# Kernel optimization log

Measured on AMD Instinct MI355X. Metric: run time of the kernel, lower is better.

Reference implementation:

```python
import jax, jax.numpy as jnp
import numpy as np

N_NODES = 50000
N_EDGES = 800000
NFEAT = 128
NHID = 128
BN_EPS = 1e-5


def setup_inputs() -> dict:
    key = jax.random.key(0)
    ks = jax.random.split(key, 8)
    x = jax.random.normal(ks[0], (N_NODES, NFEAT), dtype=jnp.float32)
    edge_index = jax.random.randint(ks[1], (2, N_EDGES), 0, N_NODES, dtype=jnp.int64)
    # Linear weights in torch layout [out, in]; scaled like kaiming-ish init.
    W1 = jax.random.normal(ks[2], (NHID, NFEAT), dtype=jnp.float32) / np.sqrt(NFEAT)
    b1 = jax.random.normal(ks[3], (NHID,), dtype=jnp.float32) * 0.01
    gamma = jnp.ones((NHID,), dtype=jnp.float32)
    beta = jnp.zeros((NHID,), dtype=jnp.float32)
    W2 = jax.random.normal(ks[4], (NHID, NHID), dtype=jnp.float32) / np.sqrt(NHID)
    b2 = jax.random.normal(ks[5], (NHID,), dtype=jnp.float32) * 0.01
    return {"x": x, "edge_index": edge_index, "W1": W1, "b1": b1,
            "gamma": gamma, "beta": beta, "W2": W2, "b2": b2}


def reference(x, edge_index, W1, b1, gamma, beta, W2, b2):
    # GINConv, eps = 0: h = (1 + eps) * x + sum_{j in N(i)} x_j
    src, dst = edge_index[0], edge_index[1]
    agg = x + jax.ops.segment_sum(x[src], dst, num_segments=N_NODES)  # [N, nfeat]
    # MLP: Linear -> ReLU -> BatchNorm1d (training stats) -> Linear
    h = jnp.maximum(agg @ W1.T + b1, 0.0)                             # [N, nhid]
    mean = jnp.mean(h, axis=0)
    var = jnp.var(h, axis=0)  # biased variance, as torch BN uses for normalization
    h = (h - mean) * jax.lax.rsqrt(var + BN_EPS) * gamma + beta
    return h @ W2.T + b2
```

## Files before the change

### kernel.cpp

```cpp
#include <hip/hip_runtime.h>

#define N_NODES 50000
#define N_EDGES 800000
#define NF 128
#define BN_EPS 1e-5f
#define G_ROWS 32
#define GBLOCKS ((N_NODES + G_ROWS - 1) / G_ROWS)
#define NB 1568
#define AP 136
#define HP 132
#define CAP 32
#define OVFCAP 8192

typedef __attribute__((ext_vector_type(8))) short short8;
typedef __attribute__((ext_vector_type(4))) float f32x4;

__device__ __forceinline__ unsigned short f2bf(float f) {
    union { float f; unsigned int i; } v; v.f = f;
    unsigned int r = (v.i + 0x7fffu + ((v.i >> 16) & 1u)) >> 16;
    return (unsigned short)r;
}
__device__ __forceinline__ float bf2f(unsigned short u) {
    union { unsigned int i; float f; } v; v.i = ((unsigned int)u) << 16; return v.f;
}
__device__ __forceinline__ float bflo(unsigned int u) { return bf2f((unsigned short)(u & 0xffffu)); }
__device__ __forceinline__ float bfhi(unsigned int u) { return bf2f((unsigned short)(u >> 16)); }

#define SETUP_C (N_NODES * NF / 4)
#define SETUP_P (128 * 128)

__global__ void scatter_build(const int* __restrict__ ei,
                              int* __restrict__ counts, int* __restrict__ ovfcnt,
                              int* __restrict__ ovf, int* __restrict__ bucket,
                              const float* __restrict__ x, unsigned short* __restrict__ xb,
                              const float* __restrict__ W1, const float* __restrict__ W2,
                              unsigned short* __restrict__ Wb1, unsigned short* __restrict__ Wb2,
                              int do_convert) {
    int i = blockIdx.x * blockDim.x + threadIdx.x;
    if (!do_convert && i >= N_EDGES) i += SETUP_C;
    if (i < N_EDGES) {
        int dst = ei[N_EDGES + i];
        int src = ei[i];
        int k = atomicAdd(&counts[dst], 1);
        if (k < CAP) {
            bucket[dst * CAP + k] = src;
        } else {
            int o = atomicAdd(ovfcnt, 1);
            if (o < OVFCAP) { ovf[2 * o] = dst; ovf[2 * o + 1] = src; }
        }
    } else if (i < N_EDGES + SETUP_C) {
        int j = i - N_EDGES;
        float4 v = ((const float4*)x)[j];
        ushort4 u;
        u.x = f2bf(v.x); u.y = f2bf(v.y); u.z = f2bf(v.z); u.w = f2bf(v.w);
        ((ushort4*)xb)[j] = u;
    } else if (i < N_EDGES + SETUP_C + SETUP_P) {
        int j = i - N_EDGES - SETUP_C;
        Wb1[j] = f2bf(W1[j]);
        Wb2[j] = f2bf(W2[j]);
    }
}

__global__ __launch_bounds__(256, 6) void fused_gather_gemm1_bf16(
    const unsigned short* __restrict__ xb,
    const int* __restrict__ counts,
    const int* __restrict__ bucket,
    const int* __restrict__ ovfcnt,
    const int* __restrict__ ovf,
    const unsigned short* __restrict__ Wb,
    const float* __restrict__ b1,
    unsigned short* __restrict__ buf,
    float* __restrict__ P) {
    __shared__ __align__(16) char smem[G_ROWS * HP * 4];
    unsigned short (*At)[AP] = (unsigned short (*)[AP])smem;
    float (*Ht)[HP] = (float (*)[HP])smem;

    int t = threadIdx.x;
    int wave = t >> 6, lane = t & 63;
    int base = blockIdx.x * G_ROWS;
    int nrows = N_NODES - base; if (nrows > G_ROWS) nrows = G_ROWS;

    const unsigned int* x2 = (const unsigned int*)xb;
    int novf = *ovfcnt; if (novf > OVFCAP) novf = OVFCAP;

    for (int nn = 0; nn < 8; nn++) {
        int r = wave * 8 + nn;
        int node = base + r;
        unsigned int packed = 0u;
        if (node < N_NODES) {
            unsigned int u = x2[(size_t)node * 64 + lane];
            float ax = bflo(u), ay = bfhi(u);
            int deg = counts[node];
            int cnt = deg < CAP ? deg : CAP;
            const int* bkt = bucket + (size_t)node * CAP;
            int e = 0;
            for (; e + 15 < cnt; e += 16) {
                unsigned int uu[16];
#pragma unroll
                for (int k = 0; k < 16; k++) uu[k] = x2[(size_t)bkt[e + k] * 64 + lane];
#pragma unroll
                for (int k = 0; k < 16; k++) { ax += bflo(uu[k]); ay += bfhi(uu[k]); }
            }
            for (; e + 3 < cnt; e += 4) {
                unsigned int u0 = x2[(size_t)bkt[e] * 64 + lane];
                unsigned int u1 = x2[(size_t)bkt[e + 1] * 64 + lane];
                unsigned int u2 = x2[(size_t)bkt[e + 2] * 64 + lane];
                unsigned int u3 = x2[(size_t)bkt[e + 3] * 64 + lane];
                ax += bflo(u0) + bflo(u1) + bflo(u2) + bflo(u3);
                ay += bfhi(u0) + bfhi(u1) + bfhi(u2) + bfhi(u3);
            }
            for (; e < cnt; e++) {
                unsigned int u0 = x2[(size_t)bkt[e] * 64 + lane];
                ax += bflo(u0);
                ay += bfhi(u0);
            }
            if (deg > CAP) {
                for (int o = 0; o < novf; o++) {
                    if (ovf[2 * o] == node) {
                        unsigned int u0 = x2[(size_t)ovf[2 * o + 1] * 64 + lane];
                        ax += bflo(u0);
                        ay += bfhi(u0);
                    }
                }
            }
            packed = ((unsigned int)f2bf(ay) << 16) | (unsigned int)f2bf(ax);
        }
        ((unsigned int*)&At[r][0])[lane] = packed;
    }
    __syncthreads();

    int m0 = (wave & 1) * 16;
    int n0 = (wave >> 1) * 64;
    int l15 = lane & 15, q = lane >> 4;

    f32x4 acc[4];
#pragma unroll
    for (int i = 0; i < 4; i++) acc[i] = (f32x4){0.f, 0.f, 0.f, 0.f};

#pragma unroll
    for (int kc = 0; kc < 4; kc++) {
        short8 a = *((const short8*)&At[m0 + l15][kc * 32 + q * 8]);
#pragma unroll
        for (int tile = 0; tile < 4; tile++) {
            short8 b = *((const short8*)(Wb + (size_t)(n0 + 16 * tile + l15) * 128 + kc * 32 + q * 8));
            acc[tile] = __builtin_amdgcn_mfma_f32_16x16x32_bf16(a, b, acc[tile], 0, 0, 0);
        }
    }
    __syncthreads();

#pragma unroll
    for (int tile = 0; tile < 4; tile++) {
        int col = n0 + 16 * tile + l15;
        float bias = b1[col];
#pragma unroll
        for (int reg = 0; reg < 4; reg++) {
            int row = q * 4 + reg;
            Ht[m0 + row][col] = fmaxf(acc[tile][reg] + bias, 0.f);
        }
    }
    __syncthreads();

    for (int i = t; i < G_ROWS * 32; i += 256) {
        int r = i >> 5, c4 = i & 31;
        int row = base + r;
        if (row < N_NODES) {
            float4 v = *((const float4*)&Ht[r][c4 * 4]);
            ushort4 u;
            u.x = f2bf(v.x); u.y = f2bf(v.y); u.z = f2bf(v.z); u.w = f2bf(v.w);
            *((ushort4*)(buf + (size_t)row * NF + c4 * 4)) = u;
        }
    }

    {
        int f = t & 127;
        bool issq = (t >= 128);
        float s = 0.f;
        for (int r = 0; r < nrows; r++) {
            float v = Ht[r][f];
            s += issq ? v * v : v;
        }
        P[(size_t)t * NB + blockIdx.x] = s;
    }
}

__global__ __launch_bounds__(256) void bn_reduce(const float* __restrict__ P,
                                                 const float* __restrict__ gamma,
                                                 const float* __restrict__ beta,
                                                 float* __restrict__ ab) {
    __shared__ float s1[256], s2[256];
    int f = blockIdx.x;
    int j = threadIdx.x;
    float a = 0.f, b = 0.f;
    for (int k = j; k < GBLOCKS; k += 256) {
        a += P[(size_t)f * NB + k];
        b += P[(size_t)(128 + f) * NB + k];
    }
    s1[j] = a; s2[j] = b;
    __syncthreads();
    for (int off = 128; off > 0; off >>= 1) {
        if (j < off) { s1[j] += s1[j + off]; s2[j] += s2[j + off]; }
        __syncthreads();
    }
    if (j == 0) {
        float mean = s1[0] * (1.0f / N_NODES);
        float var = s2[0] * (1.0f / N_NODES) - mean * mean;
        float rstd = rsqrtf(var + BN_EPS);
        float aa = gamma[f] * rstd;
        float cc = beta[f] - mean * aa;
        ab[f] = aa;
        ab[128 + f] = cc;
    }
}

__global__ __launch_bounds__(256) void gemm2_bf16(
    const unsigned short* __restrict__ buf,
    const unsigned short* __restrict__ Wb,
    const float* __restrict__ b2,
    const float* __restrict__ ab,
    float* __restrict__ out) {
    __shared__ __align__(16) char smem[G_ROWS * HP * 4];
    unsigned short (*At)[AP] = (unsigned short (*)[AP])smem;
    float (*Ht)[HP] = (float (*)[HP])smem;

    int t = threadIdx.x;
    int base = blockIdx.x * G_ROWS;
    int nrows = N_NODES - base; if (nrows > G_ROWS) nrows = G_ROWS;

    for (int i = t; i < G_ROWS * 32; i += 256) {
        int r = i >> 5, c4 = i & 31;
        ushort4 u = make_ushort4(0, 0, 0, 0);
        if (r < nrows) {
            ushort4 hv = *((const ushort4*)(buf + (size_t)(base + r) * NF + c4 * 4));
            float4 av = ((const float4*)ab)[c4];
            float4 cv = ((const float4*)(ab + 128))[c4];
            u.x = f2bf(bf2f(hv.x) * av.x + cv.x);
            u.y = f2bf(bf2f(hv.y) * av.y + cv.y);
            u.z = f2bf(bf2f(hv.z) * av.z + cv.z);
            u.w = f2bf(bf2f(hv.w) * av.w + cv.w);
        }
        *((ushort4*)&At[r][c4 * 4]) = u;
    }
    __syncthreads();

    int wave = t >> 6, lane = t & 63;
    int m0 = (wave & 1) * 16;
    int n0 = (wave >> 1) * 64;
    int l15 = lane & 15, q = lane >> 4;

    f32x4 acc[4];
#pragma unroll
    for (int i = 0; i < 4; i++) acc[i] = (f32x4){0.f, 0.f, 0.f, 0.f};

#pragma unroll
    for (int kc = 0; kc < 4; kc++) {
        short8 a = *((const short8*)&At[m0 + l15][kc * 32 + q * 8]);
#pragma unroll
        for (int tile = 0; tile < 4; tile++) {
            short8 b = *((const short8*)(Wb + (size_t)(n0 + 16 * tile + l15) * 128 + kc * 32 + q * 8));
            acc[tile] = __builtin_amdgcn_mfma_f32_16x16x32_bf16(a, b, acc[tile], 0, 0, 0);
        }
    }
    __syncthreads();

#pragma unroll
    for (int tile = 0; tile < 4; tile++) {
        int col = n0 + 16 * tile + l15;
        float bias = b2[col];
#pragma unroll
        for (int reg = 0; reg < 4; reg++) {
            int row = q * 4 + reg;
            Ht[m0 + row][col] = acc[tile][reg] + bias;
        }
    }
    __syncthreads();

    for (int i = t; i < G_ROWS * 32; i += 256) {
        int r = i >> 5, c4 = i & 31;
        int row = base + r;
        if (row < N_NODES)
            *((float4*)(out + (size_t)row * NF + c4 * 4)) = *((const float4*)&Ht[r][c4 * 4]);
    }
}

__global__ void finalize_bn(const float* __restrict__ stats,
                            const float* __restrict__ gamma,
                            const float* __restrict__ beta,
                            float* __restrict__ ab) {
    int f = threadIdx.x;
    if (f < 128) {
        float mean = stats[f] * (1.0f / N_NODES);
        float var = stats[128 + f] * (1.0f / N_NODES) - mean * mean;
        float rstd = rsqrtf(var + BN_EPS);
        float a = gamma[f] * rstd;
        float c = beta[f] - mean * a;
        ab[f] = a;
        ab[128 + f] = c;
    }
}

__global__ __launch_bounds__(256) void fused_gather_gemm1_f32(
    const float* __restrict__ xv,
    const int* __restrict__ counts,
    const int* __restrict__ bucket,
    const int* __restrict__ ovfcnt,
    const int* __restrict__ ovf,
    const unsigned short* __restrict__ Wb,
    const float* __restrict__ b1,
    float* __restrict__ hout,
    float* __restrict__ stats) {
    __shared__ unsigned short At[G_ROWS][AP];
    __shared__ float Ht[G_ROWS][HP];

    int t = threadIdx.x;
    int wave = t >> 6, lane = t & 63;
    int base = blockIdx.x * G_ROWS;
    int nrows = N_NODES - base; if (nrows > G_ROWS) nrows = G_ROWS;

    const float2* xf2 = (const float2*)xv;
    int novf = *ovfcnt; if (novf > OVFCAP) novf = OVFCAP;

    for (int nn = 0; nn < 8; nn++) {
        int r = wave * 8 + nn;
        int node = base + r;
        float2 acc = make_float2(0.f, 0.f);
        if (node < N_NODES) {
            acc = xf2[(size_t)node * 64 + lane];
            int deg = counts[node];
            int cnt = deg < CAP ? deg : CAP;
            const int* bkt = bucket + (size_t)node * CAP;
            for (int e = 0; e < cnt; e++) {
                float2 v0 = xf2[(size_t)bkt[e] * 64 + lane];
                acc.x += v0.x;
                acc.y += v0.y;
            }
            if (deg > CAP) {
                for (int o = 0; o < novf; o++) {
                    if (ovf[2 * o] == node) {
                        float2 v0 = xf2[(size_t)ovf[2 * o + 1] * 64 + lane];
                        acc.x += v0.x;
                        acc.y += v0.y;
                    }
                }
            }
        }
        unsigned int packed = ((unsigned int)f2bf(acc.y) << 16) | (unsigned int)f2bf(acc.x);
        *((unsigned int*)&At[r][lane * 2]) = packed;
    }
    __syncthreads();

    int m0 = (wave & 1) * 16;
    int n0 = (wave >> 1) * 64;
    int l15 = lane & 15, q = lane >> 4;

    f32x4 acc[4];
#pragma unroll
    for (int i = 0; i < 4; i++) acc[i] = (f32x4){0.f, 0.f, 0.f, 0.f};

#pragma unroll
    for (int kc = 0; kc < 4; kc++) {
        short8 a = *((const short8*)&At[m0 + l15][kc * 32 + q * 8]);
#pragma unroll
        for (int tile = 0; tile < 4; tile++) {
            short8 b = *((const short8*)(Wb + (size_t)(n0 + 16 * tile + l15) * 128 + kc * 32 + q * 8));
            acc[tile] = __builtin_amdgcn_mfma_f32_16x16x32_bf16(a, b, acc[tile], 0, 0, 0);
        }
    }

#pragma unroll
    for (int tile = 0; tile < 4; tile++) {
        int col = n0 + 16 * tile + l15;
        float bias = b1[col];
#pragma unroll
        for (int reg = 0; reg < 4; reg++) {
            int row = q * 4 + reg;
            Ht[m0 + row][col] = fmaxf(acc[tile][reg] + bias, 0.f);
        }
    }
    __syncthreads();

    for (int i = t; i < G_ROWS * 32; i += 256) {
        int r = i >> 5, c4 = i & 31;
        int row = base + r;
        if (row < N_NODES)
            *((float4*)(hout + (size_t)row * NF + c4 * 4)) = *((const float4*)&Ht[r][c4 * 4]);
    }

    if (t < 128) {
        float s = 0.f, sq = 0.f;
        for (int r = 0; r < nrows; r++) {
            float v = Ht[r][t];
            s += v; sq += v * v;
        }
        atomicAdd(&stats[t], s);
        atomicAdd(&stats[128 + t], sq);
    }
}

__global__ __launch_bounds__(256) void gemm2_f32(
    float* __restrict__ h,
    const unsigned short* __restrict__ Wb,
    const float* __restrict__ b2,
    const float* __restrict__ ab) {
    __shared__ unsigned short At[G_ROWS][AP];
    __shared__ float Ht[G_ROWS][HP];

    int t = threadIdx.x;
    int base = blockIdx.x * G_ROWS;
    int nrows = N_NODES - base; if (nrows > G_ROWS) nrows = G_ROWS;

    for (int i = t; i < G_ROWS * 32; i += 256) {
        int r = i >> 5, c4 = i & 31;
        float4 v = make_float4(0.f, 0.f, 0.f, 0.f);
        if (r < nrows) {
            float4 hv = ((const float4*)(h + (size_t)(base + r) * NF))[c4];
            float4 av = ((const float4*)ab)[c4];
            float4 cv = ((const float4*)(ab + 128))[c4];
            v.x = hv.x * av.x + cv.x;
            v.y = hv.y * av.y + cv.y;
            v.z = hv.z * av.z + cv.z;
            v.w = hv.w * av.w + cv.w;
        }
        ushort4 u;
        u.x = f2bf(v.x); u.y = f2bf(v.y); u.z = f2bf(v.z); u.w = f2bf(v.w);
        *((ushort4*)&At[r][c4 * 4]) = u;
    }
    __syncthreads();

    int wave = t >> 6, lane = t & 63;
    int m0 = (wave & 1) * 16;
    int n0 = (wave >> 1) * 64;
    int l15 = lane & 15, q = lane >> 4;

    f32x4 acc[4];
#pragma unroll
    for (int i = 0; i < 4; i++) acc[i] = (f32x4){0.f, 0.f, 0.f, 0.f};

#pragma unroll
    for (int kc = 0; kc < 4; kc++) {
        short8 a = *((const short8*)&At[m0 + l15][kc * 32 + q * 8]);
#pragma unroll
        for (int tile = 0; tile < 4; tile++) {
            short8 b = *((const short8*)(Wb + (size_t)(n0 + 16 * tile + l15) * 128 + kc * 32 + q * 8));
            acc[tile] = __builtin_amdgcn_mfma_f32_16x16x32_bf16(a, b, acc[tile], 0, 0, 0);
        }
    }

#pragma unroll
    for (int tile = 0; tile < 4; tile++) {
        int col = n0 + 16 * tile + l15;
        float bias = b2[col];
#pragma unroll
        for (int reg = 0; reg < 4; reg++) {
            int row = q * 4 + reg;
            Ht[m0 + row][col] = acc[tile][reg] + bias;
        }
    }
    __syncthreads();

    for (int i = t; i < G_ROWS * 32; i += 256) {
        int r = i >> 5, c4 = i & 31;
        int row = base + r;
        if (row < N_NODES)
            *((float4*)(h + (size_t)row * NF + c4 * 4)) = *((const float4*)&Ht[r][c4 * 4]);
    }
}

extern "C" void kernel_launch(void* const* d_in, const int* in_sizes, int n_in,
                              void* d_out, int out_size, void* d_ws, size_t ws_size,
                              hipStream_t stream) {
    const float* x     = (const float*)d_in[0];
    const int*   ei    = (const int*)d_in[1];
    const float* W1    = (const float*)d_in[2];
    const float* b1    = (const float*)d_in[3];
    const float* gamma = (const float*)d_in[4];
    const float* beta  = (const float*)d_in[5];
    const float* W2    = (const float*)d_in[6];
    const float* b2    = (const float*)d_in[7];

    float* out = (float*)d_out;

    float*          stats    = (float*)d_ws;
    float*          ab       = stats + 256;
    float*          P        = ab + 256;
    unsigned short* Wb1      = (unsigned short*)(P + 256 * NB);
    unsigned short* Wb2      = Wb1 + 128 * 128;
    int*            counts   = (int*)(Wb2 + 128 * 128);
    int*            ovfcnt   = counts + N_NODES;
    int*            ovf      = ovfcnt + 16;
    int*            bucket   = ovf + 2 * OVFCAP;
    unsigned short* xb       = (unsigned short*)(bucket + (size_t)N_NODES * CAP);
    unsigned short* buf      = xb + (size_t)N_NODES * NF;

    size_t need = (size_t)((char*)(buf + (size_t)N_NODES * NF) - (char*)d_ws);
    size_t need_fb = (size_t)((char*)xb - (char*)d_ws);
    bool bf16_path = ws_size >= need;

    if (bf16_path) {
        hipMemsetAsync(counts, 0, (N_NODES + 16) * sizeof(int), stream);
        int total = N_EDGES + SETUP_C + SETUP_P;
        scatter_build<<<(total + 255) / 256, 256, 0, stream>>>(
            ei, counts, ovfcnt, ovf, bucket, x, xb, W1, W2, Wb1, Wb2, 1);
        fused_gather_gemm1_bf16<<<GBLOCKS, 256, 0, stream>>>(
            xb, counts, bucket, ovfcnt, ovf, Wb1, b1, buf, P);
        bn_reduce<<<128, 256, 0, stream>>>(P, gamma, beta, ab);
        gemm2_bf16<<<GBLOCKS, 256, 0, stream>>>(buf, Wb2, b2, ab, out);
    } else if (ws_size >= need_fb) {
        hipMemsetAsync(counts, 0, (N_NODES + 16) * sizeof(int), stream);
        hipMemsetAsync(stats, 0, 256 * sizeof(float), stream);
        int total = N_EDGES + SETUP_P;
        scatter_build<<<(total + 255) / 256, 256, 0, stream>>>(
            ei, counts, ovfcnt, ovf, bucket, x, (unsigned short*)0, W1, W2, Wb1, Wb2, 0);
        fused_gather_gemm1_f32<<<GBLOCKS, 256, 0, stream>>>(
            x, counts, bucket, ovfcnt, ovf, Wb1, b1, out, stats);
        finalize_bn<<<1, 128, 0, stream>>>(stats, gamma, beta, ab);
        gemm2_f32<<<GBLOCKS, 256, 0, stream>>>(out, Wb2, b2, ab);
    }
}
```

Before: 219.8 us.

## Slice edge scatter by destination range and fold BN reduction into gemm1 last block

The scatter kernel now uses 1024 blocks, each handling one of 8 destination-node slices and re-reading all edges but only inserting those whose destination falls in its slice. This is meant to localise atomics and bucket writes so each slice stays cache-resident. A separate 512-block grid-stride section converts x and the weights to bf16. The bn_reduce kernel is removed: the last gemm1 block, detected with a done-counter atomic, reduces the per-block partial sums and writes the BN scale and shift. This saves a launch but serialises the final reduction onto a single block, and each edge index is now read 8 times.

```diff
diff --git a/kernel.cpp b/kernel.cpp
--- a/kernel.cpp
+++ b/kernel.cpp
@@ -11,6 +11,11 @@
 #define HP 132
 #define CAP 32
 #define OVFCAP 8192
+#define NSLICE 8
+#define SLICE_N (N_NODES / NSLICE)
+#define SC_BLK 1024
+#define CV_BLK 512
+#define NCHUNK ((N_EDGES + 255) / 256)
 
 typedef __attribute__((ext_vector_type(8))) short short8;
 typedef __attribute__((ext_vector_type(4))) float f32x4;
@@ -29,35 +34,52 @@
 #define SETUP_C (N_NODES * NF / 4)
 #define SETUP_P (128 * 128)
 
-__global__ void scatter_build(const int* __restrict__ ei,
-                              int* __restrict__ counts, int* __restrict__ ovfcnt,
-                              int* __restrict__ ovf, int* __restrict__ bucket,
-                              const float* __restrict__ x, unsigned short* __restrict__ xb,
-                              const float* __restrict__ W1, const float* __restrict__ W2,
-                              unsigned short* __restrict__ Wb1, unsigned short* __restrict__ Wb2,
-                              int do_convert) {
-    int i = blockIdx.x * blockDim.x + threadIdx.x;
-    if (!do_convert && i >= N_EDGES) i += SETUP_C;
-    if (i < N_EDGES) {
-        int dst = ei[N_EDGES + i];
-        int src = ei[i];
-        int k = atomicAdd(&counts[dst], 1);
-        if (k < CAP) {
-            bucket[dst * CAP + k] = src;
-        } else {
-            int o = atomicAdd(ovfcnt, 1);
-            if (o < OVFCAP) { ovf[2 * o] = dst; ovf[2 * o + 1] = src; }
-        }
-    } else if (i < N_EDGES + SETUP_C) {
-        int j = i - N_EDGES;
-        float4 v = ((const float4*)x)[j];
-        ushort4 u;
-        u.x = f2bf(v.x); u.y = f2bf(v.y); u.z = f2bf(v.z); u.w = f2bf(v.w);
-        ((ushort4*)xb)[j] = u;
-    } else if (i < N_EDGES + SETUP_C + SETUP_P) {
-        int j = i - N_EDGES - SETUP_C;
-        Wb1[j] = f2bf(W1[j]);
-        Wb2[j] = f2bf(W2[j]);
+__global__ __launch_bounds__(256) void scatter_build(
+    const int* __restrict__ ei,
+    int* __restrict__ counts, int* __restrict__ ovfcnt,
+    int* __restrict__ ovf, int* __restrict__ bucket,
+    const float* __restrict__ x, unsigned short* __restrict__ xb,
+    const float* __restrict__ W1, const float* __restrict__ W2,
+    unsigned short* __restrict__ Wb1, unsigned short* __restrict__ Wb2,
+    int do_convert) {
+    int b = blockIdx.x;
+    int t = threadIdx.x;
+    if (b < SC_BLK) {
+        int sl = b & 7;
+        int g = b >> 3;
+        int lo = sl * SLICE_N;
+        int hi = lo + SLICE_N;
+        for (int chunk = g; chunk < NCHUNK; chunk += SC_BLK / 8) {
+            int e = chunk * 256 + t;
+            if (e < N_EDGES) {
+                int dst = ei[N_EDGES + e];
+                int src = ei[e];
+                if (dst >= lo && dst < hi) {
+                    int k = atomicAdd(&counts[dst], 1);
+                    if (k < CAP) {
+                        bucket[dst * CAP + k] = src;
+                    } else {
+                        int o = atomicAdd(ovfcnt, 1);
+                        if (o < OVFCAP) { ovf[2 * o] = dst; ovf[2 * o + 1] = src; }
+                    }
+                }
+            }
+        }
+    } else {
+        int i0 = (b - SC_BLK) * 256 + t;
+        int stride = CV_BLK * 256;
+        if (do_convert) {
+            for (int i = i0; i < SETUP_C; i += stride) {
+                float4 v = ((const float4*)x)[i];
+                ushort4 u;
+                u.x = f2bf(v.x); u.y = f2bf(v.y); u.z = f2bf(v.z); u.w = f2bf(v.w);
+                ((ushort4*)xb)[i] = u;
+            }
+        }
+        for (int i = i0; i < SETUP_P; i += stride) {
+            Wb1[i] = f2bf(W1[i]);
+            Wb2[i] = f2bf(W2[i]);
+        }
     }
 }
 
@@ -69,11 +91,17 @@
     const int* __restrict__ ovf,
     const unsigned short* __restrict__ Wb,
     const float* __restrict__ b1,
+    const float* __restrict__ gamma,
+    const float* __restrict__ beta,
     unsigned short* __restrict__ buf,
-    float* __restrict__ P) {
+    float* __restrict__ P,
+    float* __restrict__ ab,
+    int* __restrict__ done) {
     __shared__ __align__(16) char smem[G_ROWS * HP * 4];
     unsigned short (*At)[AP] = (unsigned short (*)[AP])smem;
     float (*Ht)[HP] = (float (*)[HP])smem;
+    float* sred = (float*)smem;
+    __shared__ int slast;
 
     int t = threadIdx.x;
     int wave = t >> 6, lane = t & 63;
@@ -181,34 +209,33 @@
         }
         P[(size_t)t * NB + blockIdx.x] = s;
     }
-}
-
-__global__ __launch_bounds__(256) void bn_reduce(const float* __restrict__ P,
-                                                 const float* __restrict__ gamma,
-                                                 const float* __restrict__ beta,
-                                                 float* __restrict__ ab) {
-    __shared__ float s1[256], s2[256];
-    int f = blockIdx.x;
-    int j = threadIdx.x;
-    float a = 0.f, b = 0.f;
-    for (int k = j; k < GBLOCKS; k += 256) {
-        a += P[(size_t)f * NB + k];
-        b += P[(size_t)(128 + f) * NB + k];
-    }
-    s1[j] = a; s2[j] = b;
-    __syncthreads();
-    for (int off = 128; off > 0; off >>= 1) {
-        if (j < off) { s1[j] += s1[j + off]; s2[j] += s2[j + off]; }
+
+    __threadfence();
+    __syncthreads();
+    if (t == 0) slast = (atomicAdd(done, 1) == (int)gridDim.x - 1);
+    __syncthreads();
+    if (slast) {
+        __threadfence();
+        const float* row = P + (size_t)t * NB;
+        float4 a0 = make_float4(0.f, 0.f, 0.f, 0.f);
+        int k = 0;
+        for (; k + 3 < GBLOCKS; k += 4) {
+            float4 v = *((const float4*)(row + k));
+            a0.x += v.x; a0.y += v.y; a0.z += v.z; a0.w += v.w;
+        }
+        float s = a0.x + a0.y + a0.z + a0.w;
+        for (; k < GBLOCKS; k++) s += row[k];
         __syncthreads();
-    }
-    if (j == 0) {
-        float mean = s1[0] * (1.0f / N_NODES);
-        float var = s2[0] * (1.0f / N_NODES) - mean * mean;
-        float rstd = rsqrtf(var + BN_EPS);
-        float aa = gamma[f] * rstd;
-        float cc = beta[f] - mean * aa;
-        ab[f] = aa;
-        ab[128 + f] = cc;
+        sred[t] = s;
+        __syncthreads();
+        if (t < 128) {
+            float mean = sred[t] * (1.0f / N_NODES);
+            float var = sred[128 + t] * (1.0f / N_NODES) - mean * mean;
+            float rstd = rsqrtf(var + BN_EPS);
+            float aa = gamma[t] * rstd;
+            ab[t] = aa;
+            ab[128 + t] = beta[t] - mean * aa;
+        }
     }
 }
 
@@ -497,18 +524,15 @@
 
     if (bf16_path) {
         hipMemsetAsync(counts, 0, (N_NODES + 16) * sizeof(int), stream);
-        int total = N_EDGES + SETUP_C + SETUP_P;
-        scatter_build<<<(total + 255) / 256, 256, 0, stream>>>(
+        scatter_build<<<SC_BLK + CV_BLK, 256, 0, stream>>>(
             ei, counts, ovfcnt, ovf, bucket, x, xb, W1, W2, Wb1, Wb2, 1);
         fused_gather_gemm1_bf16<<<GBLOCKS, 256, 0, stream>>>(
-            xb, counts, bucket, ovfcnt, ovf, Wb1, b1, buf, P);
-        bn_reduce<<<128, 256, 0, stream>>>(P, gamma, beta, ab);
+            xb, counts, bucket, ovfcnt, ovf, Wb1, b1, gamma, beta, buf, P, ab, ovfcnt + 1);
         gemm2_bf16<<<GBLOCKS, 256, 0, stream>>>(buf, Wb2, b2, ab, out);
     } else if (ws_size >= need_fb) {
         hipMemsetAsync(counts, 0, (N_NODES + 16) * sizeof(int), stream);
         hipMemsetAsync(stats, 0, 256 * sizeof(float), stream);
-        int total = N_EDGES + SETUP_P;
-        scatter_build<<<(total + 255) / 256, 256, 0, stream>>>(
+        scatter_build<<<SC_BLK + CV_BLK, 256, 0, stream>>>(
             ei, counts, ovfcnt, ovf, bucket, x, (unsigned short*)0, W1, W2, Wb1, Wb2, 0);
         fused_gather_gemm1_f32<<<GBLOCKS, 256, 0, stream>>>(
             x, counts, bucket, ovfcnt, ovf, Wb1, b1, out, stats);
```

After: 436.6 us. 1.99x slower.
